# Performance work log

Hardware: AMD Instinct MI355X
Metric: run time of the kernel (lower is better)

Reference implementation:

```python
import jax, jax.numpy as jnp
import numpy as np


def _conv3x3(x, w):
    # NCHW input, OIHW weight, stride 1, padding 1 (SAME for 3x3)
    return jax.lax.conv_general_dilated(
        x, w, window_strides=(1, 1), padding=((1, 1), (1, 1)),
        dimension_numbers=('NCHW', 'OIHW', 'NCHW'))


def _conv1x1(x, w):
    return jax.lax.conv_general_dilated(
        x, w, window_strides=(1, 1), padding=((0, 0), (0, 0)),
        dimension_numbers=('NCHW', 'OIHW', 'NCHW'))


def setup_inputs() -> dict:
    key = jax.random.key(0)
    k_x, k_w1, k_w2, k_wm = jax.random.split(key, 4)
    N, C, H, W = 16, 256, 64, 64
    fan = C * 9
    x = jax.random.normal(k_x, (N, C, H, W), dtype=jnp.float32)
    w1 = jax.random.normal(k_w1, (C, C, 3, 3), dtype=jnp.float32) * (2.0 / fan) ** 0.5
    w2 = jax.random.normal(k_w2, (C, C, 3, 3), dtype=jnp.float32) * (2.0 / fan) ** 0.5
    w_mask = jax.random.normal(k_wm, (1, C, 1, 1), dtype=jnp.float32) * (1.0 / C) ** 0.5
    b_mask = jnp.zeros((1,), dtype=jnp.float32)
    return {'x': x, 'w1': w1, 'w2': w2, 'w_mask': w_mask, 'b_mask': b_mask}


def reference(x, w1, w2, w_mask, b_mask):
    # MaskUnit: 1x1 conv -> logits -> hard binary mask (straight-through estimator)
    logits = _conv1x1(x, w_mask) + b_mask[None, :, None, None]  # [N,1,H,W]
    hard = (logits > 0).astype(x.dtype)
    mask = logits + jax.lax.stop_gradient(hard - logits)        # std mask, binary in fwd
    # dilated mask: 3x3 max-pool (covers 3x3 receptive field of active outputs)
    mask_dilate = jax.lax.reduce_window(
        mask, -jnp.inf, jax.lax.max, (1, 1, 3, 3), (1, 1, 1, 1), 'SAME')
    # sparse branch: conv1 gated by dilated mask, conv2 gated by std mask
    h = jax.nn.relu(_conv3x3(x, w1) * mask_dilate)
    h = jax.nn.relu(_conv3x3(h, w2) * mask)
    # apply_mask + residual (mask binary -> h*mask == h already, kept for fidelity)
    out = x + h * mask
    return out
```

## Files before the change

### kernel.cpp

```cpp
#include <hip/hip_runtime.h>
#include <hip/hip_bf16.h>

#define C_ 256
#define H_ 64
#define W_ 64
#define N_ 16
#define HW_ 4096
#define IMG_ (C_ * HW_)
#define PADIMG_ (66 * 66 * 256)
#define WT_ELEMS_ (9 * 16 * 256 * 16)

typedef short bf16x8 __attribute__((ext_vector_type(8)));
typedef float f32x16 __attribute__((ext_vector_type(16)));

__device__ __forceinline__ unsigned short f2bf(float f) {
  __hip_bfloat16 h = __float2bfloat16(f);
  return *reinterpret_cast<unsigned short*>(&h);
}

__device__ __forceinline__ void gld_lds16(const void* g, void* l) {
  __builtin_amdgcn_global_load_lds(
      (const __attribute__((address_space(1))) void*)g,
      (__attribute__((address_space(3))) void*)l, 16, 0, 0);
}

__global__ __launch_bounds__(256) void xpadmask_kernel(
    const float* __restrict__ x, const float* __restrict__ wm,
    const float* __restrict__ bm, short* __restrict__ Xp,
    unsigned char* __restrict__ mask) {
  __shared__ unsigned short lds[64 * 260];
  __shared__ double dsum[16][64];
  __shared__ float wms[256];
  const int h = blockIdx.x, img = blockIdx.y;
  const int tid = threadIdx.x;
  const int pxq = tid & 15, cg = tid >> 4;
  const int p0 = pxq * 4;
  wms[tid] = wm[tid];
  __syncthreads();
  const float* xi = x + (size_t)img * IMG_ + h * 64;
  double s0 = 0.0, s1 = 0.0, s2 = 0.0, s3 = 0.0;
#pragma unroll
  for (int i = 0; i < 16; ++i) {
    const int c = cg * 16 + i;
    const float4 v = *(const float4*)&xi[(size_t)c * HW_ + p0];
    lds[(p0 + 0) * 260 + c] = f2bf(v.x);
    lds[(p0 + 1) * 260 + c] = f2bf(v.y);
    lds[(p0 + 2) * 260 + c] = f2bf(v.z);
    lds[(p0 + 3) * 260 + c] = f2bf(v.w);
    const double wmc = (double)wms[c];
    s0 += (double)v.x * wmc;
    s1 += (double)v.y * wmc;
    s2 += (double)v.z * wmc;
    s3 += (double)v.w * wmc;
  }
  dsum[cg][p0 + 0] = s0;
  dsum[cg][p0 + 1] = s1;
  dsum[cg][p0 + 2] = s2;
  dsum[cg][p0 + 3] = s3;
  __syncthreads();
  short* Xpimg = Xp + (size_t)img * PADIMG_;
  short* Xpi = Xpimg + ((h + 1) * 66 + 1) * 256;
  const int wv = tid >> 6, wl = tid & 63;
#pragma unroll
  for (int j = 0; j < 16; ++j) {
    int w = j * 4 + wv;
    int c4 = wl * 4;
    uint2 d = *(const uint2*)&lds[w * 260 + c4];
    *(uint2*)&Xpi[(size_t)w * 256 + c4] = d;
  }
  if (tid < 128) {
    const int side = tid >> 6;
    const int e = (tid & 63) * 4;
    *(uint2*)&Xpimg[((size_t)(h + 1) * 66 + side * 65) * 256 + e] =
        make_uint2(0u, 0u);
  }
  if (h == 0 || h == 63) {
    uint2* rowp = (uint2*)(Xpimg + (size_t)((h == 0) ? 0 : 65) * 66 * 256);
    for (int o = tid; o < 66 * 256 / 4; o += 256) rowp[o] = make_uint2(0u, 0u);
  }
  if (tid < 64) {
    double t = (double)bm[0];
#pragma unroll
    for (int g = 0; g < 16; ++g) t += dsum[g][tid];
    mask[img * HW_ + h * 64 + tid] = (t > 0.0) ? 1 : 0;
  }
}

__global__ __launch_bounds__(256) void wt_halo_kernel(
    const float* __restrict__ w1, const float* __restrict__ w2,
    short* __restrict__ Wt1, short* __restrict__ Wt2,
    short* __restrict__ Hp) {
  const int bx = blockIdx.x;
  const int tid = threadIdx.x;
  if (bx < 512) {
    const int k = bx & 255, which = bx >> 8;
    const float* src = which ? w2 : w1;
    short* dst = which ? Wt2 : Wt1;
    const float* s = src + ((size_t)k * 256 + tid) * 9;
    const int kc = tid >> 4, ce = tid & 15;
#pragma unroll
    for (int t = 0; t < 9; ++t)
      dst[(((size_t)t * 16 + kc) * 256 + k) * 16 + ce] = (short)f2bf(s[t]);
  } else {
    const int img = bx - 512;
    short* Hpi = Hp + (size_t)img * PADIMG_;
    for (int q = tid; q < 260 * 32; q += 256) {
      const int p = q >> 5, seg = q & 31;
      int r, c;
      if (p < 66) { r = 0; c = p; }
      else if (p < 132) { r = 65; c = p - 66; }
      else if (p < 196) { r = p - 131; c = 0; }
      else { r = p - 195; c = 65; }
      uint4* d = (uint4*)(Hpi + (size_t)(r * 66 + c) * 256);
      d[seg] = make_uint4(0u, 0u, 0u, 0u);
    }
  }
}

#define BBUF 10560
#define WOFF 21120
#define WBUF 9216

__device__ __forceinline__ void stage_BW(short* sm, int buf, const short* Xb,
                                         const short* Wg, int ch0, int kc,
                                         int wave, int lane) {
  short* Bd = sm + buf * BBUF;
  short* Wd = sm + WOFF + buf * WBUF;
  const int ko = kc * 16;
#pragma unroll
  for (int q = 0; q < 10; ++q) {
    const int n = wave + 4 * q;
    if (n < 22) {
      const int h = (n >= 11) ? 1 : 0;
      const int i = n - h * 11;
      const int row0 = (i < 10) ? i * 64 : 596;
      gld_lds16(Xb + (size_t)(row0 + lane) * 256 + ko + h * 8,
                Bd + h * 5280 + row0 * 8);
    } else {
      const int m = n - 22;
      const int t = m >> 1, ih = m & 1;
      gld_lds16(Wg + (((size_t)t * 16 + kc) * 256 + ch0 + ih * 32 +
                      (lane & 31)) * 16 + (lane >> 5) * 8,
                Wd + (t * 2 + ih) * 512);
    }
  }
}

template <int EPI>
__global__ __launch_bounds__(256, 2) void conv_mfma(
    const short* __restrict__ src, const short* __restrict__ Wt,
    const unsigned char* __restrict__ gate, const float* __restrict__ xres,
    short* __restrict__ dstH, float* __restrict__ dstF, int swz) {
  __shared__ __align__(16) short sm[2 * BBUF + 2 * WBUF];

  const int tid = threadIdx.x;
  const int lane = tid & 63, wave = tid >> 6;
  const int ln31 = lane & 31, kh = lane >> 5;

  int bx, by, bz;
  {
    int d = blockIdx.x + 4 * (blockIdx.y + 8 * blockIdx.z);
    if (swz) {
      int k = d & 7, j = d >> 3;
      bx = j & 3;
      by = (j >> 2) & 7;
      bz = ((j >> 5) << 3) + k;
    } else {
      bx = blockIdx.x;
      by = blockIdx.y;
      bz = blockIdx.z;
    }
  }
  const int ch0 = bx * 64;
  const int h0 = by * 8;
  const int img = bz;

  const short* Xb = src + (size_t)img * PADIMG_ + (size_t)(h0 * 66) * 256;

  f32x16 acc[2][4];
#pragma unroll
  for (int i = 0; i < 2; ++i)
#pragma unroll
    for (int j = 0; j < 4; ++j)
#pragma unroll
      for (int e = 0; e < 16; ++e) acc[i][j][e] = 0.f;

  stage_BW(sm, 0, Xb, Wt, ch0, 0, wave, lane);
  asm volatile("s_waitcnt vmcnt(0)\n\ts_barrier" ::: "memory");

  for (int kk = 0; kk < 16; ++kk) {
    const int cur = kk & 1;
    if (kk < 15) stage_BW(sm, cur ^ 1, Xb, Wt, ch0, kk + 1, wave, lane);

    const short* Bth = sm + cur * BBUF + kh * 5280 + (wave * 132 + ln31) * 8;
    const short* Wth = sm + WOFF + cur * WBUF + (kh * 32 + ln31) * 8;

    bf16x8 ac[2], bc[4], an[2], bn[4];
#pragma unroll
    for (int i = 0; i < 2; ++i)
      ac[i] = *(const bf16x8*)(Wth + i * 512);
#pragma unroll
    for (int j = 0; j < 4; ++j)
      bc[j] = *(const bf16x8*)(Bth + ((j >> 1) * 66 + (j & 1) * 32) * 8);

#pragma unroll
    for (int t = 0; t < 9; ++t) {
      if (t < 8) {
        const int dy = (t + 1) / 3, dx = (t + 1) % 3;
#pragma unroll
        for (int i = 0; i < 2; ++i)
          an[i] = *(const bf16x8*)(Wth + ((t + 1) * 2 + i) * 512);
#pragma unroll
        for (int j = 0; j < 4; ++j)
          bn[j] = *(const bf16x8*)(Bth +
                                   (((j >> 1) + dy) * 66 + (j & 1) * 32 + dx) * 8);
      }
      __builtin_amdgcn_s_setprio(1);
#pragma unroll
      for (int j = 0; j < 4; ++j) {
        acc[0][j] = __builtin_amdgcn_mfma_f32_32x32x16_bf16(ac[0], bc[j],
                                                            acc[0][j], 0, 0, 0);
        acc[1][j] = __builtin_amdgcn_mfma_f32_32x32x16_bf16(ac[1], bc[j],
                                                            acc[1][j], 0, 0, 0);
      }
      __builtin_amdgcn_s_setprio(0);
      if (t < 8) {
#pragma unroll
        for (int i = 0; i < 2; ++i) ac[i] = an[i];
#pragma unroll
        for (int j = 0; j < 4; ++j) bc[j] = bn[j];
      }
    }
    if (kk < 15)
      asm volatile("s_waitcnt vmcnt(0)\n\ts_barrier" ::: "memory");
  }

  const int rb = h0 + wave * 2;
#pragma unroll
  for (int j = 0; j < 4; ++j) {
    const int r = rb + (j >> 1);
    const int col = (j & 1) * 32 + ln31;
    const int pidx = r * 64 + col;
    unsigned int g;
    if (EPI == 0) {
      g = 0;
#pragma unroll
      for (int dy = -1; dy <= 1; ++dy) {
        const int rr = r + dy;
        if (rr < 0 || rr >= H_) continue;
#pragma unroll
        for (int dx = -1; dx <= 1; ++dx) {
          const int cc = col + dx;
          if (cc < 0 || cc >= W_) continue;
          g |= gate[img * HW_ + rr * W_ + cc];
        }
      }
    } else {
      g = gate[img * HW_ + pidx];
    }
#pragma unroll
    for (int i = 0; i < 2; ++i) {
      const f32x16 v = acc[i][j];
#pragma unroll
      for (int rg = 0; rg < 4; ++rg) {
        const int ch = ch0 + i * 32 + rg * 8 + kh * 4;
        float e0 = g ? fmaxf(v[rg * 4 + 0], 0.f) : 0.f;
        float e1 = g ? fmaxf(v[rg * 4 + 1], 0.f) : 0.f;
        float e2 = g ? fmaxf(v[rg * 4 + 2], 0.f) : 0.f;
        float e3 = g ? fmaxf(v[rg * 4 + 3], 0.f) : 0.f;
        if (EPI == 0) {
          uint2 u;
          u.x = (unsigned int)f2bf(e0) | ((unsigned int)f2bf(e1) << 16);
          u.y = (unsigned int)f2bf(e2) | ((unsigned int)f2bf(e3) << 16);
          short* dp = dstH + (size_t)img * PADIMG_ +
                      ((size_t)((r + 1) * 66 + (col + 1))) * 256 + ch;
          *(uint2*)dp = u;
        } else {
          size_t o = (size_t)img * IMG_ + (size_t)ch * HW_ + pidx;
          dstF[o] = xres[o] + e0;
          dstF[o + HW_] = xres[o + HW_] + e1;
          dstF[o + 2 * HW_] = xres[o + 2 * HW_] + e2;
          dstF[o + 3 * HW_] = xres[o + 3 * HW_] + e3;
        }
      }
    }
  }
}

extern "C" void kernel_launch(void* const* d_in, const int* in_sizes, int n_in,
                              void* d_out, int out_size, void* d_ws,
                              size_t ws_size, hipStream_t stream) {
  const float* x = (const float*)d_in[0];
  const float* w1 = (const float*)d_in[1];
  const float* w2 = (const float*)d_in[2];
  const float* wmask = (const float*)d_in[3];
  const float* bmask = (const float*)d_in[4];
  float* out = (float*)d_out;

  char* ws = (char*)d_ws;
  unsigned char* mask = (unsigned char*)ws;
  short* Wt1 = (short*)(ws + 65536);
  short* Wt2 = Wt1 + WT_ELEMS_;
  const size_t fixed = 65536 + 4 * (size_t)WT_ELEMS_;
  short* Xp = (short*)(ws + fixed);

  const size_t tailpad = 32768;
  const size_t per_img = 2 * (size_t)PADIMG_ * 2;
  int B = (ws_size > fixed + tailpad)
              ? (int)((ws_size - fixed - tailpad) / per_img) : 0;
  if (B > N_) B = N_;
  if (B < 1) B = 1;
  short* Hp = Xp + (size_t)B * PADIMG_;

  wt_halo_kernel<<<512 + B, 256, 0, stream>>>(w1, w2, Wt1, Wt2, Hp);

  for (int n0 = 0; n0 < N_; n0 += B) {
    const int nb = (N_ - n0 < B) ? (N_ - n0) : B;
    const int swz = (nb % 8 == 0) ? 1 : 0;
    xpadmask_kernel<<<dim3(64, nb), 256, 0, stream>>>(
        x + (size_t)n0 * IMG_, wmask, bmask, Xp, mask + n0 * HW_);
    conv_mfma<0><<<dim3(4, 8, nb), 256, 0, stream>>>(
        Xp, Wt1, mask + n0 * HW_, nullptr, Hp, nullptr, swz);
    conv_mfma<1><<<dim3(4, 8, nb), 256, 0, stream>>>(
        Hp, Wt2, mask + n0 * HW_, x + (size_t)n0 * IMG_, nullptr,
        out + (size_t)n0 * IMG_, swz);
  }
}
```

Before: 284.6 us.

## Fuse all stages into one cooperative persistent kernel with grid syncs

Replaces the sequence of launches (weight transform, pad/mask, conv1, conv2 per image batch) with a single cooperative kernel of 512 blocks that runs every stage and separates them with grid-wide syncs. Each stage is factored into a device function so the old multi-launch path remains as a fallback if the cooperative launch fails. This removes launch gaps and tail effects between kernels, but it requires all 512 blocks to be co-resident, turns the epilogue selector into a runtime flag instead of a template parameter, and adds grid-sync cost plus idle blocks whenever a batch has fewer than 512 work units.

```diff
diff --git a/kernel.cpp b/kernel.cpp
--- a/kernel.cpp
+++ b/kernel.cpp
@@ -1,5 +1,8 @@
 #include <hip/hip_runtime.h>
 #include <hip/hip_bf16.h>
+#include <hip/hip_cooperative_groups.h>
+
+namespace cg = cooperative_groups;
 
 #define C_ 256
 #define H_ 64
@@ -24,20 +27,21 @@
       (__attribute__((address_space(3))) void*)l, 16, 0, 0);
 }
 
-__global__ __launch_bounds__(256) void xpadmask_kernel(
-    const float* __restrict__ x, const float* __restrict__ wm,
+__device__ __forceinline__ void xpad_unit(
+    const float* __restrict__ xn, const float* __restrict__ wm,
     const float* __restrict__ bm, short* __restrict__ Xp,
-    unsigned char* __restrict__ mask) {
-  __shared__ unsigned short lds[64 * 260];
-  __shared__ double dsum[16][64];
-  __shared__ float wms[256];
-  const int h = blockIdx.x, img = blockIdx.y;
+    unsigned char* __restrict__ mn, int u, short* smraw) {
+  unsigned short* lds = (unsigned short*)smraw;
+  double* dsum = (double*)((char*)smraw + 33280);
+  float* wms = (float*)((char*)smraw + 41472);
+  const int h = u & 63, img = u >> 6;
   const int tid = threadIdx.x;
   const int pxq = tid & 15, cg = tid >> 4;
   const int p0 = pxq * 4;
+  __syncthreads();
   wms[tid] = wm[tid];
   __syncthreads();
-  const float* xi = x + (size_t)img * IMG_ + h * 64;
+  const float* xi = xn + (size_t)img * IMG_ + h * 64;
   double s0 = 0.0, s1 = 0.0, s2 = 0.0, s3 = 0.0;
 #pragma unroll
   for (int i = 0; i < 16; ++i) {
@@ -53,13 +57,12 @@
     s2 += (double)v.z * wmc;
     s3 += (double)v.w * wmc;
   }
-  dsum[cg][p0 + 0] = s0;
-  dsum[cg][p0 + 1] = s1;
-  dsum[cg][p0 + 2] = s2;
-  dsum[cg][p0 + 3] = s3;
+  dsum[cg * 64 + p0 + 0] = s0;
+  dsum[cg * 64 + p0 + 1] = s1;
+  dsum[cg * 64 + p0 + 2] = s2;
+  dsum[cg * 64 + p0 + 3] = s3;
   __syncthreads();
-  short* Xpimg = Xp + (size_t)img * PADIMG_;
-  short* Xpi = Xpimg + ((h + 1) * 66 + 1) * 256;
+  short* Xpi = Xp + (size_t)img * PADIMG_ + ((h + 1) * 66 + 1) * 256;
   const int wv = tid >> 6, wl = tid & 63;
 #pragma unroll
   for (int j = 0; j < 16; ++j) {
@@ -68,6 +71,23 @@
     uint2 d = *(const uint2*)&lds[w * 260 + c4];
     *(uint2*)&Xpi[(size_t)w * 256 + c4] = d;
   }
+  if (tid < 64) {
+    double t = (double)bm[0];
+#pragma unroll
+    for (int g = 0; g < 16; ++g) t += dsum[g * 64 + tid];
+    mn[img * HW_ + h * 64 + tid] = (t > 0.0) ? 1 : 0;
+  }
+}
+
+__global__ __launch_bounds__(256) void xpadmask_kernel(
+    const float* __restrict__ x, const float* __restrict__ wm,
+    const float* __restrict__ bm, short* __restrict__ Xp,
+    unsigned char* __restrict__ mask) {
+  __shared__ __align__(16) short smx[21248];
+  const int h = blockIdx.x, img = blockIdx.y;
+  const int tid = threadIdx.x;
+  xpad_unit(x, wm, bm, Xp, mask, img * 64 + h, smx);
+  short* Xpimg = Xp + (size_t)img * PADIMG_;
   if (tid < 128) {
     const int side = tid >> 6;
     const int e = (tid & 63) * 4;
@@ -77,12 +97,6 @@
   if (h == 0 || h == 63) {
     uint2* rowp = (uint2*)(Xpimg + (size_t)((h == 0) ? 0 : 65) * 66 * 256);
     for (int o = tid; o < 66 * 256 / 4; o += 256) rowp[o] = make_uint2(0u, 0u);
-  }
-  if (tid < 64) {
-    double t = (double)bm[0];
-#pragma unroll
-    for (int g = 0; g < 16; ++g) t += dsum[g][tid];
-    mask[img * HW_ + h * 64 + tid] = (t > 0.0) ? 1 : 0;
   }
 }
 
@@ -146,30 +160,24 @@
   }
 }
 
-template <int EPI>
-__global__ __launch_bounds__(256, 2) void conv_mfma(
-    const short* __restrict__ src, const short* __restrict__ Wt,
+__device__ __forceinline__ void conv_unit(
+    int d, int swz, const short* __restrict__ src, const short* __restrict__ Wt,
     const unsigned char* __restrict__ gate, const float* __restrict__ xres,
-    short* __restrict__ dstH, float* __restrict__ dstF, int swz) {
-  __shared__ __align__(16) short sm[2 * BBUF + 2 * WBUF];
-
+    short* __restrict__ dstH, float* __restrict__ dstF, int epi, short* sm) {
   const int tid = threadIdx.x;
   const int lane = tid & 63, wave = tid >> 6;
   const int ln31 = lane & 31, kh = lane >> 5;
 
   int bx, by, bz;
-  {
-    int d = blockIdx.x + 4 * (blockIdx.y + 8 * blockIdx.z);
-    if (swz) {
-      int k = d & 7, j = d >> 3;
-      bx = j & 3;
-      by = (j >> 2) & 7;
-      bz = ((j >> 5) << 3) + k;
-    } else {
-      bx = blockIdx.x;
-      by = blockIdx.y;
-      bz = blockIdx.z;
-    }
+  if (swz) {
+    int k = d & 7, j = d >> 3;
+    bx = j & 3;
+    by = (j >> 2) & 7;
+    bz = ((j >> 5) << 3) + k;
+  } else {
+    bx = d & 3;
+    by = (d >> 2) & 7;
+    bz = d >> 5;
   }
   const int ch0 = bx * 64;
   const int h0 = by * 8;
@@ -242,7 +250,7 @@
     const int col = (j & 1) * 32 + ln31;
     const int pidx = r * 64 + col;
     unsigned int g;
-    if (EPI == 0) {
+    if (epi == 0) {
       g = 0;
 #pragma unroll
       for (int dy = -1; dy <= 1; ++dy) {
@@ -268,7 +276,7 @@
         float e1 = g ? fmaxf(v[rg * 4 + 1], 0.f) : 0.f;
         float e2 = g ? fmaxf(v[rg * 4 + 2], 0.f) : 0.f;
         float e3 = g ? fmaxf(v[rg * 4 + 3], 0.f) : 0.f;
-        if (EPI == 0) {
+        if (epi == 0) {
           uint2 u;
           u.x = (unsigned int)f2bf(e0) | ((unsigned int)f2bf(e1) << 16);
           u.y = (unsigned int)f2bf(e2) | ((unsigned int)f2bf(e3) << 16);
@@ -287,6 +295,72 @@
   }
 }
 
+template <int EPI>
+__global__ __launch_bounds__(256, 2) void conv_mfma(
+    const short* __restrict__ src, const short* __restrict__ Wt,
+    const unsigned char* __restrict__ gate, const float* __restrict__ xres,
+    short* __restrict__ dstH, float* __restrict__ dstF, int swz) {
+  __shared__ __align__(16) short sm[2 * BBUF + 2 * WBUF];
+  const int d = blockIdx.x + 4 * (blockIdx.y + 8 * blockIdx.z);
+  conv_unit(d, swz, src, Wt, gate, xres, dstH, dstF, EPI, sm);
+}
+
+__global__ __launch_bounds__(256, 2) void mega(
+    const float* __restrict__ x, const float* __restrict__ w1,
+    const float* __restrict__ w2, const float* __restrict__ wm,
+    const float* __restrict__ bm, float* __restrict__ out,
+    unsigned char* __restrict__ mask, short* __restrict__ Wt1,
+    short* __restrict__ Wt2, short* __restrict__ Xp, short* __restrict__ Hp,
+    int B) {
+  __shared__ __align__(16) short sm[2 * BBUF + 2 * WBUF];
+  cg::grid_group grid = cg::this_grid();
+  const int b = blockIdx.x;
+  const int tid = threadIdx.x;
+
+  {
+    const int k = b & 255, which = b >> 8;
+    const float* src = which ? w2 : w1;
+    short* dst = which ? Wt2 : Wt1;
+    const float* s = src + ((size_t)k * 256 + tid) * 9;
+    const int kc = tid >> 4, ce = tid & 15;
+#pragma unroll
+    for (int t = 0; t < 9; ++t)
+      dst[(((size_t)t * 16 + kc) * 256 + k) * 16 + ce] = (short)f2bf(s[t]);
+    if (b < 2 * B) {
+      short* buf = (b < B) ? (Hp + (size_t)b * PADIMG_)
+                           : (Xp + (size_t)(b - B) * PADIMG_);
+      for (int q = tid; q < 260 * 32; q += 256) {
+        const int p = q >> 5, seg = q & 31;
+        int r, c;
+        if (p < 66) { r = 0; c = p; }
+        else if (p < 132) { r = 65; c = p - 66; }
+        else if (p < 196) { r = p - 131; c = 0; }
+        else { r = p - 195; c = 65; }
+        uint4* dd = (uint4*)(buf + (size_t)(r * 66 + c) * 256);
+        dd[seg] = make_uint4(0u, 0u, 0u, 0u);
+      }
+    }
+  }
+  grid.sync();
+
+  for (int n0 = 0; n0 < N_; n0 += B) {
+    const int nb = (N_ - n0 < B) ? (N_ - n0) : B;
+    const int swz = (nb % 8 == 0) ? 1 : 0;
+    const float* xn = x + (size_t)n0 * IMG_;
+    unsigned char* mn = mask + n0 * HW_;
+
+    for (int u = b; u < 64 * nb; u += 512) xpad_unit(xn, wm, bm, Xp, mn, u, sm);
+    grid.sync();
+    if (b < 32 * nb)
+      conv_unit(b, swz, Xp, Wt1, mn, nullptr, Hp, nullptr, 0, sm);
+    grid.sync();
+    if (b < 32 * nb)
+      conv_unit(b, swz, Hp, Wt2, mn, xn, nullptr, out + (size_t)n0 * IMG_, 1,
+                sm);
+    grid.sync();
+  }
+}
+
 extern "C" void kernel_launch(void* const* d_in, const int* in_sizes, int n_in,
                               void* d_out, int out_size, void* d_ws,
                               size_t ws_size, hipStream_t stream) {
@@ -312,8 +386,14 @@
   if (B < 1) B = 1;
   short* Hp = Xp + (size_t)B * PADIMG_;
 
+  void* kargs[] = {(void*)&x,    (void*)&w1,  (void*)&w2,  (void*)&wmask,
+                   (void*)&bmask, (void*)&out, (void*)&mask, (void*)&Wt1,
+                   (void*)&Wt2,  (void*)&Xp,  (void*)&Hp,  (void*)&B};
+  hipError_t err = hipLaunchCooperativeKernel(
+      (const void*)mega, dim3(512), dim3(256), kargs, 0, stream);
+  if (err == hipSuccess) return;
+
   wt_halo_kernel<<<512 + B, 256, 0, stream>>>(w1, w2, Wt1, Wt2, Hp);
-
   for (int n0 = 0; n0 < N_; n0 += B) {
     const int nb = (N_ - n0 < B) ? (N_ - n0) : B;
     const int swz = (nb % 8 == 0) ? 1 : 0;
```

After: 651.8 us. 129% more time.
